# Kernel optimization log

Measured on AMD Instinct MI355X. Metric: run time of the kernel, lower is better.

Reference implementation:

```python
import jax, jax.numpy as jnp
import numpy as np

B, C, CI, H, W = 16, 256, 128, 64, 64


def setup_inputs() -> dict:
    key = jax.random.key(0)
    k1, k2, k3, k4, k5, k6 = jax.random.split(key, 6)
    x_gallery = jax.random.normal(k1, (B, C, H, W), dtype=jnp.float32)
    x_query = jax.random.normal(k2, (B, C, H, W), dtype=jnp.float32)
    # 1x1 conv weights (kernel_size=1 -> equivalent to per-pixel linear map)
    s = 1.0 / np.sqrt(C)
    theta_w = jax.random.uniform(k3, (CI, C), jnp.float32, -s, s)
    theta_b = jax.random.uniform(k4, (CI,), jnp.float32, -s, s)
    phi_w = jax.random.uniform(k5, (CI, C), jnp.float32, -s, s)
    phi_b = jax.random.uniform(k6, (CI,), jnp.float32, -s, s)
    return {"x_gallery": x_gallery, "x_query": x_query,
            "theta_w": theta_w, "theta_b": theta_b,
            "phi_w": phi_w, "phi_b": phi_b}


def reference(x_gallery, x_query, theta_w, theta_b, phi_w, phi_b):
    b, c, h, w = x_gallery.shape
    # 1x1 convs == channel-mixing einsum
    theta_x = jnp.einsum('bchw,oc->bohw', x_gallery, theta_w) + theta_b[None, :, None, None]
    phi_x = jnp.einsum('bchw,oc->bohw', x_query, phi_w) + phi_b[None, :, None, None]
    t = theta_x.reshape(b, theta_x.shape[1], -1)   # [B, CI, HW]
    p = phi_x.reshape(b, phi_x.shape[1], -1)       # [B, CI, H'W']
    n = p.shape[-1]
    # f[b, i, j] = <theta[:, i], phi[:, j]> / N   (norm == 'size')
    f = jnp.einsum('bci,bcj->bij', t, p) / n       # [B, HW, H'W']
    f = jnp.max(f, axis=2)                         # row-wise max (non-softmax attention)
    f = f.reshape(b, 1, h, w)
    return jax.nn.sigmoid(f)                       # message == 'attention_map'
```

## Files before the change

kernel.cpp:

```cpp
#include <hip/hip_runtime.h>
#include <hip/hip_bf16.h>

#define B_   16
#define CIN  256
#define CO   128
#define HW   4096

typedef __attribute__((ext_vector_type(8))) short short8;
typedef __attribute__((ext_vector_type(4))) float f32x4;
typedef __attribute__((ext_vector_type(4))) unsigned u32x4;

__device__ __forceinline__ short f32_to_bf16_rne(float f) {
    union { float f; unsigned u; } v; v.f = f;
    unsigned u = v.u;
    u += 0x7fffu + ((u >> 16) & 1u);
    return (short)(u >> 16);
}

__global__ __launch_bounds__(256) void wconv_kernel(
    const float* __restrict__ tw, const float* __restrict__ pw,
    short* __restrict__ wbf)
{
    const int idx = blockIdx.x * 256 + threadIdx.x;
    const float v = (idx < CO * CIN) ? tw[idx] : pw[idx - CO * CIN];
    wbf[idx] = f32_to_bf16_rne(v);
}

__global__ __launch_bounds__(256, 4) void proj_kernel(
    const float* __restrict__ xg, const float* __restrict__ xq,
    const float* __restrict__ tb, const float* __restrict__ pb,
    const short* __restrict__ wbf,
    short* __restrict__ tT, short* __restrict__ pT)
{
    const int n     = blockIdx.x;
    const int xcd   = n & 7;
    const int q     = n >> 3;
    const int itile = q & 63;
    const int rr    = q >> 6;
    const int which = rr & 1;
    const int b     = xcd + 8 * (rr >> 1);

    const float* x    = which ? xq : xg;
    const float* bias = which ? pb : tb;
    const short* wb   = wbf + which * CO * CIN;
    short*       out  = which ? pT : tT;

    const int i0   = itile * 64;
    const int tid  = threadIdx.x;
    const int lane = tid & 63;
    const int wv   = tid >> 6;
    const int nrow = lane & 15;
    const int quad = lane >> 4;

    const int si   = tid & 63;
    const int cig  = tid >> 6;

    __shared__ __align__(16) short xT[2][64][64];

    f32x4 acc[4][2] = {};

    float bias_v[2];
    bias_v[0] = bias[wv * 32 + 0  + nrow];
    bias_v[1] = bias[wv * 32 + 16 + nrow];

    const float* xb = x + (long)b * CIN * HW + i0 + si;

    float fst[2][8];
    auto stage_load = [&](int c) {
        const float* src = xb + (long)(c * 64) * HW;
        #pragma unroll
        for (int ro = 0; ro < 2; ro++)
            #pragma unroll
            for (int r = 0; r < 8; r++)
                fst[ro][r] = src[(long)((ro * 4 + cig) * 8 + r) * HW];
    };
    auto stage_write = [&](int buf) {
        #pragma unroll
        for (int ro = 0; ro < 2; ro++) {
            u32x4 d;
            #pragma unroll
            for (int p = 0; p < 4; p++) {
                const unsigned lo = (unsigned short)f32_to_bf16_rne(fst[ro][2 * p]);
                const unsigned hi = (unsigned short)f32_to_bf16_rne(fst[ro][2 * p + 1]);
                d[p] = lo | (hi << 16);
            }
            const int ck = (ro * 4 + cig) ^ (si & 7);
            *(u32x4*)&xT[buf][si][ck * 8] = d;
        }
    };

    short8 wf[2][2][2];
    auto wload = [&](int c, int buf) {
        #pragma unroll
        for (int ks = 0; ks < 2; ks++)
            #pragma unroll
            for (int nt = 0; nt < 2; nt++)
                wf[buf][ks][nt] = *(const short8*)(
                    wb + (wv * 32 + nt * 16 + nrow) * CIN + c * 64 + ks * 32 + quad * 8);
    };

    auto compute = [&](int buf) {
        #pragma unroll
        for (int ks = 0; ks < 2; ks++)
            #pragma unroll
            for (int mt = 0; mt < 4; mt++) {
                const int row = mt * 16 + nrow;
                const int ck  = (ks * 4 + quad) ^ (row & 7);
                const short8 a = *(const short8*)&xT[buf][row][ck * 8];
                acc[mt][0] = __builtin_amdgcn_mfma_f32_16x16x32_bf16(a, wf[buf][ks][0], acc[mt][0], 0, 0, 0);
                acc[mt][1] = __builtin_amdgcn_mfma_f32_16x16x32_bf16(a, wf[buf][ks][1], acc[mt][1], 0, 0, 0);
            }
    };

    wload(0, 0);
    stage_load(0);
    stage_write(0);
    #pragma unroll
    for (int c = 0; c < 4; c++) {
        __syncthreads();
        if (c < 3) { stage_load(c + 1); wload(c + 1, (c + 1) & 1); }
        compute(c & 1);
        if (c < 3) stage_write((c + 1) & 1);
    }

    #pragma unroll
    for (int mt = 0; mt < 4; mt++)
        #pragma unroll
        for (int nt = 0; nt < 2; nt++) {
            const int co = wv * 32 + nt * 16 + nrow;
            #pragma unroll
            for (int r = 0; r < 4; r++) {
                const int il = mt * 16 + quad * 4 + r;
                out[((long)b * HW + i0 + il) * CO + co] =
                    f32_to_bf16_rne(acc[mt][nt][r] + bias_v[nt]);
            }
        }
}

__global__ __launch_bounds__(256, 2) void maxgemm_kernel(
    const short* __restrict__ tT, const short* __restrict__ pT,
    float* __restrict__ pmax)
{
    const int n     = blockIdx.x;
    const int b     = (n & 7) + 8 * ((n >> 3) & 1);
    const int mm    = n >> 4;
    const int itile = mm & 7;
    const int jq    = mm >> 3;
    const int i0    = itile * 512;
    const int j0    = jq * 1024;
    const int tid   = threadIdx.x;
    const int lane  = tid & 63;
    const int wv    = tid >> 6;
    const int nrow  = lane & 15;
    const int quad  = lane >> 4;

    __shared__ short bT[2][64][128];

    short8 afrag[8][4];
    {
        const short* ta = tT + ((long)b * HW + i0 + wv * 128) * CO;
        #pragma unroll
        for (int mt = 0; mt < 8; mt++)
            #pragma unroll
            for (int ks = 0; ks < 4; ks++)
                afrag[mt][ks] = *(const short8*)(ta + (mt * 16 + nrow) * CO + ks * 32 + quad * 8);
    }

    const short* pb2 = pT + (long)b * HW * CO + (long)j0 * CO;
    const int sc8 = tid & 15;
    const int sj0 = tid >> 4;

    short8 sreg[4];
    auto stage_load = [&](int jt) {
        const short* src = pb2 + (long)jt * 64 * CO;
        #pragma unroll
        for (int r = 0; r < 4; r++)
            sreg[r] = *(const short8*)(src + (sj0 + r * 16) * CO + sc8 * 8);
    };
    auto stage_write = [&](int buf) {
        #pragma unroll
        for (int r = 0; r < 4; r++) {
            const int j  = sj0 + r * 16;
            const int c8 = sc8 ^ (j & 7);
            *(short8*)&bT[buf][j][c8 * 8] = sreg[r];
        }
    };

    f32x4 vmax[8];
    #pragma unroll
    for (int mt = 0; mt < 8; mt++)
        vmax[mt] = (f32x4){-1e30f, -1e30f, -1e30f, -1e30f};

    const f32x4 kz = {0.f, 0.f, 0.f, 0.f};

    auto compute = [&](int buf) {
        #pragma unroll
        for (int np = 0; np < 2; np++) {
            short8 bf0[4], bf1[4];
            const int ja = np * 32 + nrow;
            const int jb = ja + 16;
            #pragma unroll
            for (int ks = 0; ks < 4; ks++) {
                bf0[ks] = *(const short8*)&bT[buf][ja][(((ks * 4 + quad) ^ (ja & 7)) * 8)];
                bf1[ks] = *(const short8*)&bT[buf][jb][(((ks * 4 + quad) ^ (jb & 7)) * 8)];
            }
            #pragma unroll
            for (int mt = 0; mt < 8; mt++) {
                f32x4 a0 = __builtin_amdgcn_mfma_f32_16x16x32_bf16(afrag[mt][0], bf0[0], kz, 0, 0, 0);
                f32x4 a1 = __builtin_amdgcn_mfma_f32_16x16x32_bf16(afrag[mt][0], bf1[0], kz, 0, 0, 0);
                #pragma unroll
                for (int ks = 1; ks < 4; ks++) {
                    a0 = __builtin_amdgcn_mfma_f32_16x16x32_bf16(afrag[mt][ks], bf0[ks], a0, 0, 0, 0);
                    a1 = __builtin_amdgcn_mfma_f32_16x16x32_bf16(afrag[mt][ks], bf1[ks], a1, 0, 0, 0);
                }
                #pragma unroll
                for (int r = 0; r < 4; r++)
                    vmax[mt][r] = fmaxf(fmaxf(a0[r], a1[r]), vmax[mt][r]);
            }
        }
    };

    stage_load(0);
    stage_write(0);
    for (int jt = 0; jt < 16; jt++) {
        __syncthreads();
        if (jt < 15) stage_load(jt + 1);
        compute(jt & 1);
        if (jt < 15) stage_write((jt + 1) & 1);
    }

    #pragma unroll
    for (int mt = 0; mt < 8; mt++)
        #pragma unroll
        for (int r = 0; r < 4; r++) {
            float v = vmax[mt][r];
            #pragma unroll
            for (int m = 8; m >= 1; m >>= 1)
                v = fmaxf(v, __shfl_xor(v, m, 64));
            vmax[mt][r] = v;
        }

    if (nrow == 0) {
        float* pm = pmax + (size_t)jq * (B_ * HW) + (size_t)b * HW + i0 + wv * 128;
        #pragma unroll
        for (int mt = 0; mt < 8; mt++)
            #pragma unroll
            for (int r = 0; r < 4; r++)
                pm[mt * 16 + quad * 4 + r] = vmax[mt][r];
    }
}

__global__ __launch_bounds__(256) void combine_kernel(
    const float* __restrict__ pmax, float* __restrict__ out)
{
    const int idx = blockIdx.x * 256 + threadIdx.x;
    float v = pmax[idx];
    #pragma unroll
    for (int p = 1; p < 4; p++)
        v = fmaxf(v, pmax[idx + p * (B_ * HW)]);
    v *= (1.0f / (float)HW);
    out[idx] = 1.0f / (1.0f + __expf(-v));
}

extern "C" void kernel_launch(void* const* d_in, const int* in_sizes, int n_in,
                              void* d_out, int out_size, void* d_ws, size_t ws_size,
                              hipStream_t stream) {
    const float* xg = (const float*)d_in[0];
    const float* xq = (const float*)d_in[1];
    const float* tw = (const float*)d_in[2];
    const float* tb = (const float*)d_in[3];
    const float* pw = (const float*)d_in[4];
    const float* pb = (const float*)d_in[5];
    float* out = (float*)d_out;

    short* tT  = (short*)d_ws;
    short* pT  = tT + (size_t)B_ * HW * CO;
    short* wbf = pT + (size_t)B_ * HW * CO;
    float* pmax = (float*)(wbf + 2 * CO * CIN);

    wconv_kernel<<<(2 * CO * CIN) / 256, 256, 0, stream>>>(tw, pw, wbf);
    proj_kernel<<<B_ * (HW / 64) * 2, 256, 0, stream>>>(xg, xq, tb, pb, wbf, tT, pT);
    maxgemm_kernel<<<B_ * (HW / 512) * 4, 256, 0, stream>>>(tT, pT, pmax);
    combine_kernel<<<(B_ * HW) / 256, 256, 0, stream>>>(pmax, out);
}
```

Baseline: 224.8 us.

## Vectorize projection input loads with float4 and use 128-channel LDS stages

The projection kernel now loads x with float4 reads, so each thread covers 4 pixels by 8 channels instead of scalar loads. Each stage covers 128 input channels, so the K loop drops from four stages to two, with a matching 16-way LDS swizzle and doubled weight-fragment registers. This targets global-load instruction count and the number of barriers. It doubles LDS use and lowers the occupancy hint from 4 to 3 blocks per CU.

```diff
diff --git a/kernel.cpp b/kernel.cpp
--- a/kernel.cpp
+++ b/kernel.cpp
@@ -17,6 +17,11 @@
     return (short)(u >> 16);
 }
 
+__device__ __forceinline__ unsigned pack_bf16(float lo, float hi) {
+    return (unsigned)(unsigned short)f32_to_bf16_rne(lo) |
+           ((unsigned)(unsigned short)f32_to_bf16_rne(hi) << 16);
+}
+
 __global__ __launch_bounds__(256) void wconv_kernel(
     const float* __restrict__ tw, const float* __restrict__ pw,
     short* __restrict__ wbf)
@@ -26,7 +31,7 @@
     wbf[idx] = f32_to_bf16_rne(v);
 }
 
-__global__ __launch_bounds__(256, 4) void proj_kernel(
+__global__ __launch_bounds__(256, 3) void proj_kernel(
     const float* __restrict__ xg, const float* __restrict__ xq,
     const float* __restrict__ tb, const float* __restrict__ pb,
     const short* __restrict__ wbf,
@@ -52,10 +57,11 @@
     const int nrow = lane & 15;
     const int quad = lane >> 4;
 
-    const int si   = tid & 63;
-    const int cig  = tid >> 6;
-
-    __shared__ __align__(16) short xT[2][64][64];
+    const int iq   = (tid & 15) * 4;
+    const int g    = tid >> 4;
+    const int swz  = tid & 15;
+
+    __shared__ __align__(16) short xT[2][64][128];
 
     f32x4 acc[4][2] = {};
 
@@ -63,50 +69,46 @@
     bias_v[0] = bias[wv * 32 + 0  + nrow];
     bias_v[1] = bias[wv * 32 + 16 + nrow];
 
-    const float* xb = x + (long)b * CIN * HW + i0 + si;
-
-    float fst[2][8];
+    const float* xb = x + (long)b * CIN * HW + i0;
+
+    float4 lv[8];
     auto stage_load = [&](int c) {
-        const float* src = xb + (long)(c * 64) * HW;
-        #pragma unroll
-        for (int ro = 0; ro < 2; ro++)
-            #pragma unroll
-            for (int r = 0; r < 8; r++)
-                fst[ro][r] = src[(long)((ro * 4 + cig) * 8 + r) * HW];
+        const float* src = xb + (long)(c * 128 + g * 8) * HW + iq;
+        #pragma unroll
+        for (int r = 0; r < 8; r++)
+            lv[r] = *(const float4*)(src + (long)r * HW);
     };
     auto stage_write = [&](int buf) {
-        #pragma unroll
-        for (int ro = 0; ro < 2; ro++) {
+        const int ck = (g ^ swz) * 8;
+        #pragma unroll
+        for (int k = 0; k < 4; k++) {
             u32x4 d;
-            #pragma unroll
-            for (int p = 0; p < 4; p++) {
-                const unsigned lo = (unsigned short)f32_to_bf16_rne(fst[ro][2 * p]);
-                const unsigned hi = (unsigned short)f32_to_bf16_rne(fst[ro][2 * p + 1]);
-                d[p] = lo | (hi << 16);
-            }
-            const int ck = (ro * 4 + cig) ^ (si & 7);
-            *(u32x4*)&xT[buf][si][ck * 8] = d;
-        }
-    };
-
-    short8 wf[2][2][2];
+            const float* f = (const float*)lv;
+            #pragma unroll
+            for (int p = 0; p < 4; p++)
+                d[p] = pack_bf16(f[(2 * p) * 4 + k], f[(2 * p + 1) * 4 + k]);
+            *(u32x4*)&xT[buf][iq + k][ck] = d;
+        }
+    };
+
+    short8 wf[2][4][2];
     auto wload = [&](int c, int buf) {
         #pragma unroll
-        for (int ks = 0; ks < 2; ks++)
+        for (int ks = 0; ks < 4; ks++)
             #pragma unroll
             for (int nt = 0; nt < 2; nt++)
                 wf[buf][ks][nt] = *(const short8*)(
-                    wb + (wv * 32 + nt * 16 + nrow) * CIN + c * 64 + ks * 32 + quad * 8);
+                    wb + (wv * 32 + nt * 16 + nrow) * CIN + c * 128 + ks * 32 + quad * 8);
     };
 
     auto compute = [&](int buf) {
         #pragma unroll
-        for (int ks = 0; ks < 2; ks++)
+        for (int ks = 0; ks < 4; ks++)
             #pragma unroll
             for (int mt = 0; mt < 4; mt++) {
                 const int row = mt * 16 + nrow;
-                const int ck  = (ks * 4 + quad) ^ (row & 7);
-                const short8 a = *(const short8*)&xT[buf][row][ck * 8];
+                const int ck  = ((ks * 4 + quad) ^ ((row >> 2) & 15)) * 8;
+                const short8 a = *(const short8*)&xT[buf][row][ck];
                 acc[mt][0] = __builtin_amdgcn_mfma_f32_16x16x32_bf16(a, wf[buf][ks][0], acc[mt][0], 0, 0, 0);
                 acc[mt][1] = __builtin_amdgcn_mfma_f32_16x16x32_bf16(a, wf[buf][ks][1], acc[mt][1], 0, 0, 0);
             }
@@ -115,13 +117,13 @@
     wload(0, 0);
     stage_load(0);
     stage_write(0);
-    #pragma unroll
-    for (int c = 0; c < 4; c++) {
-        __syncthreads();
-        if (c < 3) { stage_load(c + 1); wload(c + 1, (c + 1) & 1); }
-        compute(c & 1);
-        if (c < 3) stage_write((c + 1) & 1);
-    }
+    __syncthreads();
+    stage_load(1);
+    wload(1, 1);
+    compute(0);
+    stage_write(1);
+    __syncthreads();
+    compute(1);
 
     #pragma unroll
     for (int mt = 0; mt < 4; mt++)
```

Result: no change. 226.8 us (+0.9%).
